# Kernel optimization log

Measured on AMD Instinct MI355X. Metric: run time of the kernel, lower is better.

## Reference

```python
import jax, jax.numpy as jnp
import numpy as np

B, C, G = 8, 64, 65536
IN_DIM, OUT_DIM = 64, 64
SLOPE = 0.1


def setup_inputs() -> dict:
    key = jax.random.key(0)
    ks = jax.random.split(key, 5)
    features = jax.random.normal(ks[0], (B, C, G), dtype=jnp.float32)
    # Conv2d(in*2, out, 1, bias=False) weights, squeezed to [out, in*2]
    W0 = jax.random.normal(ks[1], (OUT_DIM, IN_DIM * 2), dtype=jnp.float32) * (1.0 / np.sqrt(IN_DIM * 2))
    W1 = jax.random.normal(ks[2], (OUT_DIM, OUT_DIM * 2), dtype=jnp.float32) * (1.0 / np.sqrt(OUT_DIM * 2))
    W2 = jax.random.normal(ks[3], (OUT_DIM, OUT_DIM * 2), dtype=jnp.float32) * (1.0 / np.sqrt(OUT_DIM * 2))
    W3 = jax.random.normal(ks[4], (OUT_DIM, OUT_DIM * 2), dtype=jnp.float32) * (1.0 / np.sqrt(OUT_DIM * 2))
    return {"features": features, "W0": W0, "W1": W1, "W2": W2, "W3": W3}


def _layer(x, W):
    # x: [B, C, G]; tile the first group's features and build (x, x - x0)
    x0 = x[:, :, :1]                               # [B, C, 1]
    h = jnp.concatenate([x, x - x0], axis=1)       # [B, 2C, G]
    # 1x1 conv == pointwise linear over channels
    y = jnp.einsum("oc,bcg->bog", W, h)            # [B, O, G]
    return jax.nn.leaky_relu(y, negative_slope=SLOPE)


def reference(features, W0, W1, W2, W3):
    x = features
    for W in (W0, W1, W2, W3):
        x = _layer(x, W)
    return jnp.max(x, axis=-1)                     # [B, O]
```

## Files before the change

### kernel.cpp

```cpp
#include <hip/hip_runtime.h>


#define G_TOT 65536

typedef _Float16 hf2 __attribute__((ext_vector_type(2)));
typedef _Float16 hf4 __attribute__((ext_vector_type(4)));
typedef _Float16 hf8 __attribute__((ext_vector_type(8)));
typedef float float4_ __attribute__((ext_vector_type(4)));

static __device__ __forceinline__ hf2 pkh(float x, float y) {
    return __builtin_bit_cast(hf2, __builtin_amdgcn_cvt_pkrtz(x, y));
}


__global__ __launch_bounds__(256) void ge_prep(
    const float* __restrict__ feat,
    const float* __restrict__ W0, const float* __restrict__ W1,
    const float* __restrict__ W2, const float* __restrict__ W3,
    float* __restrict__ ws)
{
    const int tid = threadIdx.x;
    const int blk = blockIdx.x;
    __shared__ float lw[64][129];
    __shared__ float x0[2][64];

    if (blk == 8) {
        unsigned* maxenc = (unsigned*)(ws + 18432);
        maxenc[tid] = 0u; maxenc[tid + 256] = 0u;
        _Float16* wf = (_Float16*)ws;
        for (int ci = tid; ci < 8192; ci += 256) {
            int f = ci >> 8, ln = (ci >> 2) & 63, h2 = ci & 3;
            int l = f >> 3, mt = (f >> 1) & 3, pr = f & 1;
            int o = (mt << 4) + (ln & 15);
            int c = (pr << 5) + ((h2 >> 1) << 4) + ((ln >> 4) << 2) + ((h2 & 1) << 1);
            const float* Wl = (l == 0) ? W0 : (l == 1) ? W1 : (l == 2) ? W2 : W3;
            float a0 = Wl[o * 128 + c]     + Wl[o * 128 + 64 + c];
            float a1 = Wl[o * 128 + c + 1] + Wl[o * 128 + 64 + c + 1];
            *(hf2*)&wf[ci << 1] = pkh(a0, a1);
        }
        return;
    }

    const int b = blk;
    if (tid < 64) x0[0][tid] = feat[(size_t)(b * 64 + tid) * G_TOT];
    float* nbias = ws + 16384;
    for (int l = 0; l < 4; ++l) {
        const float* Wl = (l == 0) ? W0 : (l == 1) ? W1 : (l == 2) ? W2 : W3;
        for (int i = tid; i < 64 * 128; i += 256) lw[i >> 7][i & 127] = Wl[i];
        __syncthreads();
        if (tid < 64) {
            const int o = tid;
            const float* src = x0[l & 1];
            float s1 = 0.f, s2 = 0.f;
            for (int c = 0; c < 64; ++c) {
                float xv = src[c];
                s1 += lw[o][c] * xv;
                s2 += lw[o][64 + c] * xv;
            }
            nbias[b * 256 + l * 64 + o] = -s2;
            x0[(l & 1) ^ 1][o] = fmaxf(s1, 0.1f * s1);
        }
        __syncthreads();
    }
}

#define COMPUTE_TILE(BF)                                                              \
    _Pragma("unroll")                                                                 \
    for (int l = 0; l < 4; ++l) {                                                     \
        float4_ acc[4];                                                               \
        _Pragma("unroll")                                                             \
        for (int mt = 0; mt < 4; ++mt) {                                              \
            if (l < 3) acc[mt] = *(const float4_*)&lbias[(l << 6) + (mt << 4) + (q << 2)]; \
            else       acc[mt] = float4_{0.f, 0.f, 0.f, 0.f};                         \
        }                                                                             \
        _Pragma("unroll")                                                             \
        for (int mt = 0; mt < 4; ++mt) {                                              \
            _Pragma("unroll")                                                         \
            for (int pr = 0; pr < 2; ++pr) {                                          \
                union { hf8 h8; hf4 h4[2]; } ua;                                      \
                ua.h8 = *(const hf8*)&lwf[((((((l << 2) + mt) << 1) + pr) << 6) + lane) << 3]; \
                acc[mt] = __builtin_amdgcn_mfma_f32_16x16x16f16(ua.h4[0], BF[(pr << 1) + 0], acc[mt], 0, 0, 0); \
                acc[mt] = __builtin_amdgcn_mfma_f32_16x16x16f16(ua.h4[1], BF[(pr << 1) + 1], acc[mt], 0, 0, 0); \
            }                                                                         \
        }                                                                             \
        if (l < 3) {                                                                  \
            _Pragma("unroll")                                                         \
            for (int mt = 0; mt < 4; ++mt) {                                          \
                union { hf2 h2[2]; hf4 h4; } u;                                       \
                u.h2[0] = pkh(acc[mt][0], acc[mt][1]);                                \
                u.h2[1] = pkh(acc[mt][2], acc[mt][3]);                                \
                hf4 h = u.h4;                                                         \
                h = __builtin_elementwise_max(h, h * k01);                            \
                BF[mt] = h;                                                           \
            }                                                                         \
        } else {                                                                      \
            _Pragma("unroll")                                                         \
            for (int mt = 0; mt < 4; ++mt)                                            \
                _Pragma("unroll")                                                     \
                for (int j = 0; j < 4; ++j)                                           \
                    rmax[mt][j] = fmaxf(rmax[mt][j], acc[mt][j]);                     \
        }                                                                             \
    }

__global__ __launch_bounds__(256, 2) void ge_main(
    const float* __restrict__ feat,
    const float* __restrict__ ws_wf,
    const float* __restrict__ nbias,
    unsigned* __restrict__ maxenc)
{
    __shared__ __align__(16) float stg[64][132];
    __shared__ __align__(16) _Float16 lwf[16384];
    __shared__ float lbias[256];
    __shared__ float blockmax[4][64];
    const int tid = threadIdx.x;

    const int nb = ((blockIdx.x & 7) << 6) | (blockIdx.x >> 3);
    const int b = nb >> 6;
    const int w = tid >> 6, lane = tid & 63, q = lane >> 4, n = lane & 15;

    const int srow = (w << 4) + (lane >> 5);
    const int scol = (lane & 31) << 2;
    const float* Sbase = feat + (size_t)b * 64 * G_TOT
                       + (size_t)((nb & 63) << 10) + scol;

    float4_ sbuf[8];
#pragma unroll
    for (int i = 0; i < 8; ++i)
        sbuf[i] = *(const float4_*)&Sbase[(size_t)(srow + (i << 1)) * G_TOT];

    {
        const float4_* wp = (const float4_*)ws_wf;
#pragma unroll
        for (int i = 0; i < 8; ++i)
            *(float4_*)&lwf[(tid + (i << 8)) << 3] = wp[tid + (i << 8)];
    }
    lbias[tid] = nbias[(b << 8) + tid];

    float rmax[4][4];
#pragma unroll
    for (int mt = 0; mt < 4; ++mt)
#pragma unroll
        for (int j = 0; j < 4; ++j) rmax[mt][j] = -__builtin_inff();

    const hf4 k01 = { (_Float16)0.1f, (_Float16)0.1f, (_Float16)0.1f, (_Float16)0.1f };

    __syncthreads();

#pragma unroll 1
    for (int p = 0; p < 8; ++p) {
#pragma unroll
        for (int i = 0; i < 8; ++i)
            *(float4_*)&stg[(w << 4) + (i << 1) + (lane >> 5)][scol] = sbuf[i];
        __syncthreads();
        if (p < 7) {
            const float* Sp = Sbase + ((p + 1) << 7);
#pragma unroll
            for (int i = 0; i < 8; ++i)
                sbuf[i] = *(const float4_*)&Sp[(size_t)(srow + (i << 1)) * G_TOT];
        }
        {
            hf4 bfA[4];
#pragma unroll
            for (int kf = 0; kf < 4; ++kf) {
                float f0 = stg[(kf << 4) + (q << 2) + 0][(w << 5) + n];
                float f1 = stg[(kf << 4) + (q << 2) + 1][(w << 5) + n];
                float f2 = stg[(kf << 4) + (q << 2) + 2][(w << 5) + n];
                float f3 = stg[(kf << 4) + (q << 2) + 3][(w << 5) + n];
                union { hf2 h2[2]; hf4 h4; } u;
                u.h2[0] = pkh(f0, f1); u.h2[1] = pkh(f2, f3);
                bfA[kf] = u.h4;
            }
            COMPUTE_TILE(bfA)
        }
        {
            hf4 bfB[4];
#pragma unroll
            for (int kf = 0; kf < 4; ++kf) {
                float f0 = stg[(kf << 4) + (q << 2) + 0][(w << 5) + 16 + n];
                float f1 = stg[(kf << 4) + (q << 2) + 1][(w << 5) + 16 + n];
                float f2 = stg[(kf << 4) + (q << 2) + 2][(w << 5) + 16 + n];
                float f3 = stg[(kf << 4) + (q << 2) + 3][(w << 5) + 16 + n];
                union { hf2 h2[2]; hf4 h4; } u;
                u.h2[0] = pkh(f0, f1); u.h2[1] = pkh(f2, f3);
                bfB[kf] = u.h4;
            }
            COMPUTE_TILE(bfB)
        }
        __syncthreads();
    }

#pragma unroll
    for (int mt = 0; mt < 4; ++mt)
#pragma unroll
        for (int j = 0; j < 4; ++j) {
            float v = rmax[mt][j];
            v = fmaxf(v, __shfl_xor(v, 1, 64));
            v = fmaxf(v, __shfl_xor(v, 2, 64));
            v = fmaxf(v, __shfl_xor(v, 4, 64));
            v = fmaxf(v, __shfl_xor(v, 8, 64));
            rmax[mt][j] = v;
        }
    if (n == 0) {
#pragma unroll
        for (int mt = 0; mt < 4; ++mt)
#pragma unroll
            for (int j = 0; j < 4; ++j)
                blockmax[w][(mt << 4) + (q << 2) + j] = rmax[mt][j];
    }
    __syncthreads();
    if (tid < 64) {
        float v = fmaxf(fmaxf(blockmax[0][tid], blockmax[1][tid]),
                        fmaxf(blockmax[2][tid], blockmax[3][tid]));
        unsigned s = __float_as_uint(v);
        unsigned enc = (s & 0x80000000u) ? ~s : (s | 0x80000000u);
        atomicMax(&maxenc[b * 64 + tid], enc);
    }
}

__global__ void ge_final(const unsigned* __restrict__ maxenc,
                         const float* __restrict__ nbias,
                         float* __restrict__ out)
{
    int i = threadIdx.x;
    if (i < 512) {
        unsigned u = maxenc[i];
        unsigned s = (u & 0x80000000u) ? (u ^ 0x80000000u) : ~u;
        float v = __uint_as_float(s) + nbias[((i >> 6) << 8) + 192 + (i & 63)];
        out[i] = fmaxf(v, 0.1f * v);
    }
}

extern "C" void kernel_launch(void* const* d_in, const int* in_sizes, int n_in,
                              void* d_out, int out_size, void* d_ws, size_t ws_size,
                              hipStream_t stream) {
    const float* feat = (const float*)d_in[0];
    const float* W0 = (const float*)d_in[1];
    const float* W1 = (const float*)d_in[2];
    const float* W2 = (const float*)d_in[3];
    const float* W3 = (const float*)d_in[4];
    float* ws = (float*)d_ws;
    unsigned* maxenc = (unsigned*)(ws + 18432);

    ge_prep<<<9, 256, 0, stream>>>(feat, W0, W1, W2, W3, ws);
    ge_main<<<512, 256, 0, stream>>>(feat, ws, ws + 16384, maxenc);
    ge_final<<<1, 512, 0, stream>>>(maxenc, ws + 16384, (float*)d_out);
}
```

Before: 263.2 us.

## Stage feature tiles with direct global-to-LDS loads and double buffering

Feature tiles no longer pass through registers followed by explicit LDS stores. They are now copied with global_load_lds straight into a double-buffered LDS staging area, padded to 272 floats per four-row group. The tile per iteration shrinks to 64 columns over 16 iterations, and only one barrier remains per iteration. The intent is to free the VGPRs that held the prefetch buffer, drop the LDS store instructions and overlap the next tile's load with compute. The risk is that completion of the async LDS loads may not be correctly waited on before the barrier, and the smaller per-iteration tile adds loop overhead.

```diff
diff --git a/kernel.cpp b/kernel.cpp
--- a/kernel.cpp
+++ b/kernel.cpp
@@ -102,13 +102,25 @@
         }                                                                             \
     }
 
+#define STAGE(PCOL, BUFBASE)                                                          \
+    _Pragma("unroll")                                                                 \
+    for (int j = 0; j < 4; ++j) {                                                     \
+        const int G_ = (w << 2) + j;                                                  \
+        const float* src_ = Fbase + (size_t)((G_ << 2) + (lane >> 4)) * G_TOT         \
+                          + (PCOL) + ((lane & 15) << 2);                              \
+        __builtin_amdgcn_global_load_lds(                                             \
+            (const __attribute__((address_space(1))) unsigned*)src_,                  \
+            (__attribute__((address_space(3))) unsigned*)&stg[(BUFBASE) + G_ * 272],  \
+            16, 0, 0);                                                                \
+    }
+
 __global__ __launch_bounds__(256, 2) void ge_main(
     const float* __restrict__ feat,
     const float* __restrict__ ws_wf,
     const float* __restrict__ nbias,
     unsigned* __restrict__ maxenc)
 {
-    __shared__ __align__(16) float stg[64][132];
+    __shared__ __align__(16) float stg[2 * 16 * 272];
     __shared__ __align__(16) _Float16 lwf[16384];
     __shared__ float lbias[256];
     __shared__ float blockmax[4][64];
@@ -118,16 +130,9 @@
     const int b = nb >> 6;
     const int w = tid >> 6, lane = tid & 63, q = lane >> 4, n = lane & 15;
 
-    const int srow = (w << 4) + (lane >> 5);
-    const int scol = (lane & 31) << 2;
-    const float* Sbase = feat + (size_t)b * 64 * G_TOT
-                       + (size_t)((nb & 63) << 10) + scol;
-
-    float4_ sbuf[8];
-#pragma unroll
-    for (int i = 0; i < 8; ++i)
-        sbuf[i] = *(const float4_*)&Sbase[(size_t)(srow + (i << 1)) * G_TOT];
-
+    const float* Fbase = feat + (size_t)b * 64 * G_TOT + (size_t)((nb & 63) << 10);
+
+    STAGE(0, 0)
     {
         const float4_* wp = (const float4_*)ws_wf;
 #pragma unroll
@@ -144,49 +149,25 @@
 
     const hf4 k01 = { (_Float16)0.1f, (_Float16)0.1f, (_Float16)0.1f, (_Float16)0.1f };
 
-    __syncthreads();
-
+    int curbase = 0;
 #pragma unroll 1
-    for (int p = 0; p < 8; ++p) {
-#pragma unroll
-        for (int i = 0; i < 8; ++i)
-            *(float4_*)&stg[(w << 4) + (i << 1) + (lane >> 5)][scol] = sbuf[i];
+    for (int p = 0; p < 16; ++p) {
         __syncthreads();
-        if (p < 7) {
-            const float* Sp = Sbase + ((p + 1) << 7);
-#pragma unroll
-            for (int i = 0; i < 8; ++i)
-                sbuf[i] = *(const float4_*)&Sp[(size_t)(srow + (i << 1)) * G_TOT];
-        }
-        {
-            hf4 bfA[4];
-#pragma unroll
-            for (int kf = 0; kf < 4; ++kf) {
-                float f0 = stg[(kf << 4) + (q << 2) + 0][(w << 5) + n];
-                float f1 = stg[(kf << 4) + (q << 2) + 1][(w << 5) + n];
-                float f2 = stg[(kf << 4) + (q << 2) + 2][(w << 5) + n];
-                float f3 = stg[(kf << 4) + (q << 2) + 3][(w << 5) + n];
-                union { hf2 h2[2]; hf4 h4; } u;
-                u.h2[0] = pkh(f0, f1); u.h2[1] = pkh(f2, f3);
-                bfA[kf] = u.h4;
-            }
-            COMPUTE_TILE(bfA)
-        }
-        {
-            hf4 bfB[4];
-#pragma unroll
-            for (int kf = 0; kf < 4; ++kf) {
-                float f0 = stg[(kf << 4) + (q << 2) + 0][(w << 5) + 16 + n];
-                float f1 = stg[(kf << 4) + (q << 2) + 1][(w << 5) + 16 + n];
-                float f2 = stg[(kf << 4) + (q << 2) + 2][(w << 5) + 16 + n];
-                float f3 = stg[(kf << 4) + (q << 2) + 3][(w << 5) + 16 + n];
-                union { hf2 h2[2]; hf4 h4; } u;
-                u.h2[0] = pkh(f0, f1); u.h2[1] = pkh(f2, f3);
-                bfB[kf] = u.h4;
-            }
-            COMPUTE_TILE(bfB)
-        }
-        __syncthreads();
+        if (p < 15) { STAGE((p + 1) << 6, curbase ^ 4352) }
+        hf4 bf[4];
+#pragma unroll
+        for (int kf = 0; kf < 4; ++kf) {
+            const int gb = curbase + ((kf << 2) + q) * 272 + (w << 4) + n;
+            float f0 = stg[gb];
+            float f1 = stg[gb + 64];
+            float f2 = stg[gb + 128];
+            float f3 = stg[gb + 192];
+            union { hf2 h2[2]; hf4 h4; } u;
+            u.h2[0] = pkh(f0, f1); u.h2[1] = pkh(f2, f3);
+            bf[kf] = u.h4;
+        }
+        COMPUTE_TILE(bf)
+        curbase ^= 4352;
     }
 
 #pragma unroll
```

New measurement: 219.9 us. 1.2x faster.
